# Kernel optimization log

Hardware: AMD Instinct MI355X
Metric: run time of the kernel (lower is better)

The kernel has to match this reference:

```python
import jax, jax.numpy as jnp
import numpy as np

BATCH = 2048      # rays
NINTRS = 256      # samples per ray (intersections has NINTRS+1 t-values)
VALID = 128       # valid samples per ray (mask pattern: first VALID of each ray)
NUM_ATOMS = 256   # grid.data_dim: dictionary size
SH_DIM = 9        # (sh_deg+1)^2, sh_deg=2
DATA_DIM = 3 * SH_DIM + 1  # 28: rgb SH coeffs + sigma
RESOLUTION = 256.0
WHITE_BKGD = True


def sh_basis_deg2(dirs):
    # dirs: (B, 3) -> (B, 9) real SH basis up to degree 2
    d = dirs / jnp.linalg.norm(dirs, axis=-1, keepdims=True)
    x, y, z = d[:, 0], d[:, 1], d[:, 2]
    one = jnp.ones_like(x)
    return jnp.stack([
        0.28209479177387814 * one,
        -0.4886025119029199 * y,
        0.4886025119029199 * z,
        -0.4886025119029199 * x,
        1.0925484305920792 * x * y,
        -1.0925484305920792 * y * z,
        0.31539156525252005 * (2.0 * z * z - x * x - y * y),
        -1.0925484305920792 * x * z,
        0.5462742152960396 * (x * x - y * y),
    ], axis=-1)


def setup_inputs() -> dict:
    key = jax.random.key(0)
    k1, k2, k3, k4, k5 = jax.random.split(key, 5)
    n_pts = BATCH * VALID
    queries = jax.random.normal(k1, (n_pts, NUM_ATOMS), dtype=jnp.float32) * 0.05
    atoms = jax.random.normal(k2, (NUM_ATOMS, DATA_DIM, 8), dtype=jnp.float32) * 0.1
    intrs_pts = jax.random.uniform(k3, (n_pts, 3), minval=-1.0, maxval=1.0, dtype=jnp.float32)
    deltas = jax.random.uniform(k4, (BATCH, NINTRS + 1), minval=0.01, maxval=0.05, dtype=jnp.float32)
    intersections = 2.0 + jnp.cumsum(deltas, axis=-1)  # sorted t-values per ray
    rays_d = jax.random.normal(k5, (BATCH, 3), dtype=jnp.float32)
    rays_d = rays_d / jnp.linalg.norm(rays_d, axis=-1, keepdims=True)
    # mask pattern: first VALID samples of each ray -> flat row-major indices
    b = np.arange(BATCH)[:, None]
    i = np.arange(VALID)[None, :]
    flat_idx = jnp.asarray((b * NINTRS + i).reshape(-1), dtype=jnp.int32)
    return {"queries": queries, "atoms": atoms, "intrs_pts": intrs_pts,
            "intersections": intersections, "rays_d": rays_d, "flat_idx": flat_idx}


def reference(queries, atoms, intrs_pts, intersections, rays_d, flat_idx):
    n_pts = queries.shape[0]
    # sparse-dictionary decode: (n_pts, num_atoms) @ (num_atoms, data_dim*8)
    data_masked = (queries @ atoms.reshape(NUM_ATOMS, -1)).reshape(n_pts, DATA_DIM, 8)

    # trilinear interpolation over the 8 corners (xyzs computed under no_grad)
    pts = jax.lax.stop_gradient(intrs_pts * (RESOLUTION / 2.0) + 1e-05)
    xyzs = pts - jnp.floor(pts)
    x, y, z = xyzs[:, 0], xyzs[:, 1], xyzs[:, 2]
    cx = jnp.stack([1.0 - x, x], axis=-1)  # (n, 2)
    cy = jnp.stack([1.0 - y, y], axis=-1)
    cz = jnp.stack([1.0 - z, z], axis=-1)
    w = (cx[:, :, None, None] * cy[:, None, :, None] * cz[:, None, None, :]).reshape(n_pts, 8)
    data_interp = jnp.einsum('ndc,nc->nd', data_masked, w)  # (n_pts, data_dim)

    # scatter sigma into ray-indexed buffer (masked_scatter_ equivalent)
    sigma_masked = data_interp[:, -1]
    sigma = jnp.zeros((BATCH * NINTRS,), dtype=sigma_masked.dtype).at[flat_idx].set(sigma_masked)
    sigma = jax.nn.relu(sigma.reshape(BATCH, NINTRS))

    # sigma2alpha: alpha compositing weights
    dists = (intersections[:, 1:] - intersections[:, :-1]) * jnp.linalg.norm(rays_d, axis=-1, keepdims=True)
    alpha = 1.0 - jnp.exp(-sigma * dists)
    trans = jnp.cumprod(1.0 - alpha + 1e-10, axis=-1)
    trans = jnp.concatenate([jnp.ones((BATCH, 1), dtype=alpha.dtype), trans[:, :-1]], axis=-1)
    abs_light = alpha * trans  # (batch, nintrs)

    # SH color reconstruction per masked point
    sh_mult_full = sh_basis_deg2(rays_d)                 # (batch, sh_dim)
    ray_idx = flat_idx // NINTRS
    sh_mult = sh_mult_full[ray_idx]                      # (n_pts, sh_dim)
    sh_masked = data_interp[:, :-1].reshape(n_pts, 3, SH_DIM)
    rgb_masked = jnp.sum(sh_mult[:, None, :] * sh_masked, axis=-1)  # (n_pts, 3)
    rgb = jnp.zeros((BATCH * NINTRS, 3), dtype=rgb_masked.dtype).at[flat_idx].set(rgb_masked)
    rgb = rgb.reshape(BATCH, NINTRS, 3)

    # shrgb2rgb: sigmoid + composite (+ white background)
    rgb = jax.nn.sigmoid(rgb)
    rgb = jnp.sum(abs_light[:, :, None] * rgb, axis=1)
    if WHITE_BKGD:
        rgb = rgb + (1.0 - jnp.sum(abs_light, axis=-1, keepdims=True))

    # depth_map: expected t at interval midpoints
    mids = 0.5 * (intersections[:, 1:] + intersections[:, :-1])
    depth = jnp.sum(abs_light * mids, axis=-1)
    return rgb, alpha, depth
```

## Files before the change

kernel.cpp:

```cpp
#include <hip/hip_runtime.h>
#include <hip/hip_bf16.h>
#include <math.h>

#define BATCH   2048
#define NINTRS  256
#define VALID   128
#define NATOMS  256
#define DDIM    28

typedef float  f32x4  __attribute__((ext_vector_type(4)));
typedef short  bf16x8 __attribute__((ext_vector_type(8)));

__device__ __forceinline__ unsigned short f32_to_bf16(float f) {
    unsigned int u = __float_as_uint(f);
    u = (u + 0x7FFFu + ((u >> 16) & 1u)) >> 16;
    return (unsigned short)u;
}

__global__ __launch_bounds__(256)
void build_atomsB(const float* __restrict__ atoms, unsigned short* __restrict__ ab)
{
    const int t = blockIdx.x * 256 + threadIdx.x;
    const int d = t >> 8;
    const int a = t & 255;
    const float* src = atoms + ((size_t)a * DDIM + d) * 8;
    f32x4 v0 = *(const f32x4*)(src);
    f32x4 v1 = *(const f32x4*)(src + 4);
    bf16x8 o;
    #pragma unroll
    for (int j = 0; j < 4; ++j) {
        o[j]   = (short)f32_to_bf16(v0[j]);
        o[j+4] = (short)f32_to_bf16(v1[j]);
    }
    *(bf16x8*)(ab + (size_t)t * 8) = o;
}

__global__ __launch_bounds__(256, 3)
void shdict_fused(const float* __restrict__ q,
                  const unsigned short* __restrict__ ab,
                  const float* __restrict__ ipts,
                  const float* __restrict__ intr,
                  const float* __restrict__ raysd,
                  float* __restrict__ out_rgb,
                  float* __restrict__ out_alpha,
                  float* __restrict__ out_depth)
{
    __shared__ char  bs[32 * 256 * 2];
    __shared__ float w_lds[VALID][9];
    __shared__ float pr_lds[VALID][5];

    const int ray  = blockIdx.x;
    const int tid  = threadIdx.x;
    const int lane = tid & 63;
    const int wav  = tid >> 6;

    const float rdx = raysd[ray*3+0], rdy = raysd[ray*3+1], rdz = raysd[ray*3+2];
    float px = 0.f, py = 0.f, pz = 0.f;
    if (tid < VALID) {
        const int n = ray * VALID + tid;
        px = ipts[n*3+0]*128.0f + 1e-5f;
        py = ipts[n*3+1]*128.0f + 1e-5f;
        pz = ipts[n*3+2]*128.0f + 1e-5f;
    }

    bf16x8 abv[28];
    #pragma unroll
    for (int d = 0; d < 28; ++d)
        abv[d] = *(const bf16x8*)(ab + ((size_t)(d * 256 + tid)) * 8);

    const float ss = rdx*rdx + rdy*rdy + rdz*rdz;
    const float rn = rsqrtf(ss);
    const float x = rdx*rn, y = rdy*rn, z = rdz*rn;
    float sh[9];
    sh[0] = 0.28209479177387814f;
    sh[1] = -0.4886025119029199f * y;
    sh[2] =  0.4886025119029199f * z;
    sh[3] = -0.4886025119029199f * x;
    sh[4] =  1.0925484305920792f * x * y;
    sh[5] = -1.0925484305920792f * y * z;
    sh[6] =  0.31539156525252005f * (2.0f*z*z - x*x - y*y);
    sh[7] = -1.0925484305920792f * x * z;
    sh[8] =  0.5462742152960396f * (x*x - y*y);

    {
        const int a = tid;
        float accB[3][8];
        #pragma unroll
        for (int k = 0; k < 3; ++k)
            #pragma unroll
            for (int c = 0; c < 8; ++c) accB[k][c] = 0.0f;
        #pragma unroll
        for (int d = 0; d < 27; ++d) {
            const int kp = d / 9, j = d - kp * 9;
            const float s = sh[j];
            const unsigned int* u = (const unsigned int*)&abv[d];
            #pragma unroll
            for (int i = 0; i < 4; ++i) {
                const float flo = __uint_as_float(u[i] << 16);
                const float fhi = __uint_as_float(u[i] & 0xffff0000u);
                accB[kp][2*i]   = fmaf(s, flo, accB[kp][2*i]);
                accB[kp][2*i+1] = fmaf(s, fhi, accB[kp][2*i+1]);
            }
        }
        #pragma unroll
        for (int kp = 0; kp < 3; ++kp)
            #pragma unroll
            for (int c = 0; c < 8; ++c) {
                const int col = kp*8 + c;
                unsigned byte = ((unsigned)col << 9) + ((unsigned)a << 1);
                byte ^= (unsigned)((col & 7) << 4);
                *(unsigned short*)(bs + byte) = f32_to_bf16(accB[kp][c]);
            }
        const unsigned short* sv = (const unsigned short*)&abv[27];
        #pragma unroll
        for (int c = 0; c < 8; ++c) {
            const int col = 24 + c;
            unsigned byte = ((unsigned)col << 9) + ((unsigned)a << 1);
            byte ^= (unsigned)((col & 7) << 4);
            *(unsigned short*)(bs + byte) = sv[c];
        }
    }

    if (tid < VALID) {
        const float fx = px - floorf(px);
        const float fy = py - floorf(py);
        const float fz = pz - floorf(pz);
        #pragma unroll
        for (int c = 0; c < 8; ++c) {
            const float wx = (c & 4) ? fx : 1.0f - fx;
            const float wy = (c & 2) ? fy : 1.0f - fy;
            const float wz = (c & 1) ? fz : 1.0f - fz;
            w_lds[tid][c] = wx * wy * wz;
        }
    }

    const int row  = lane & 15;
    const int kgrp = lane >> 4;
    const float* ga0 = q + (size_t)(ray*VALID + wav*32 + row) * NATOMS + kgrp*8;
    const float* ga1 = ga0 + 16 * NATOMS;

    f32x4 pf[3][4];

#define ISSUE_STEP(s, kk) do {                                                   \
    const float* _p0 = ga0 + (kk)*32;                                            \
    const float* _p1 = ga1 + (kk)*32;                                            \
    asm volatile("global_load_dwordx4 %0, %1, off" : "=v"(pf[s][0]) : "v"(_p0)   : "memory"); \
    asm volatile("global_load_dwordx4 %0, %1, off" : "=v"(pf[s][1]) : "v"(_p0+4) : "memory"); \
    asm volatile("global_load_dwordx4 %0, %1, off" : "=v"(pf[s][2]) : "v"(_p1)   : "memory"); \
    asm volatile("global_load_dwordx4 %0, %1, off" : "=v"(pf[s][3]) : "v"(_p1+4) : "memory"); \
} while (0)

    asm volatile("s_waitcnt vmcnt(0)" ::: "memory");
    ISSUE_STEP(0, 0);
    ISSUE_STEP(1, 1);
    ISSUE_STEP(2, 2);

    asm volatile("s_waitcnt lgkmcnt(0)" ::: "memory");
    __builtin_amdgcn_s_barrier();

    f32x4 acc[2][2];
    #pragma unroll
    for (int m = 0; m < 2; ++m)
        #pragma unroll
        for (int n = 0; n < 2; ++n)
            acc[m][n] = (f32x4){0.f, 0.f, 0.f, 0.f};

    #pragma unroll
    for (int ks = 0; ks < 8; ++ks) {
        if (ks <= 5)      asm volatile("s_waitcnt vmcnt(8)" ::: "memory");
        else if (ks == 6) asm volatile("s_waitcnt vmcnt(4)" ::: "memory");
        else              asm volatile("s_waitcnt vmcnt(0)" ::: "memory");
        __builtin_amdgcn_sched_barrier(0);

        const int s = ks % 3;
        bf16x8 af0, af1;
        #pragma unroll
        for (int j = 0; j < 4; ++j) {
            af0[j]   = (short)f32_to_bf16(pf[s][0][j]);
            af0[j+4] = (short)f32_to_bf16(pf[s][1][j]);
            af1[j]   = (short)f32_to_bf16(pf[s][2][j]);
            af1[j+4] = (short)f32_to_bf16(pf[s][3][j]);
        }

        if (ks + 3 < 8) ISSUE_STEP(s, ks + 3);

        bf16x8 bfrag[2];
        const int abase = ks*32 + kgrp*8;
        #pragma unroll
        for (int nt = 0; nt < 2; ++nt) {
            const int col = nt*16 + row;
            unsigned byte = ((unsigned)col << 9) + ((unsigned)abase << 1);
            byte ^= (unsigned)((col & 7) << 4);
            bfrag[nt] = *(const bf16x8*)(bs + byte);
        }

        acc[0][0] = __builtin_amdgcn_mfma_f32_16x16x32_bf16(af0, bfrag[0], acc[0][0], 0, 0, 0);
        acc[0][1] = __builtin_amdgcn_mfma_f32_16x16x32_bf16(af0, bfrag[1], acc[0][1], 0, 0, 0);
        acc[1][0] = __builtin_amdgcn_mfma_f32_16x16x32_bf16(af1, bfrag[0], acc[1][0], 0, 0, 0);
        acc[1][1] = __builtin_amdgcn_mfma_f32_16x16x32_bf16(af1, bfrag[1], acc[1][1], 0, 0, 0);
    }
#undef ISSUE_STEP

    const int cc  = lane & 7;
    const int kph = (lane & 15) >> 3;
    #pragma unroll
    for (int m = 0; m < 2; ++m) {
        const int ptb = wav*32 + m*16 + kgrp*4;
        #pragma unroll
        for (int nt = 0; nt < 2; ++nt) {
            const int kp = nt*2 + kph;
            #pragma unroll
            for (int r = 0; r < 4; ++r) {
                float t = acc[m][nt][r] * w_lds[ptb + r][cc];
                t += __shfl_xor(t, 1);
                t += __shfl_xor(t, 2);
                t += __shfl_xor(t, 4);
                if (cc == 0) pr_lds[ptb + r][kp] = t;
            }
        }
    }
    __syncthreads();

    if (wav == 0) {
        const float rnorm = sqrtf(ss);
        const int i0 = lane * 2;
        const float t0 = intr[ray*257 + i0];
        const float t1 = intr[ray*257 + i0 + 1];
        const float t2 = intr[ray*257 + i0 + 2];
        const float d0 = (t1 - t0) * rnorm;
        const float d1 = (t2 - t1) * rnorm;
        const float s0 = fmaxf(pr_lds[i0][3],     0.0f);
        const float s1 = fmaxf(pr_lds[i0 + 1][3], 0.0f);
        const float a0 = 1.0f - __expf(-s0 * d0);
        const float a1 = 1.0f - __expf(-s1 * d1);
        const float f0 = 1.0f - a0 + 1e-10f;
        const float f1 = 1.0f - a1 + 1e-10f;

        float pprod = f0 * f1;
        #pragma unroll
        for (int off = 1; off < 64; off <<= 1) {
            float v = __shfl_up(pprod, off);
            if (lane >= off) pprod *= v;
        }
        float excl = __shfl_up(pprod, 1);
        if (lane == 0) excl = 1.0f;

        const float tr0 = excl;
        const float tr1 = excl * f0;
        const float al0 = a0 * tr0;
        const float al1 = a1 * tr1;
        const float mid0 = 0.5f * (t0 + t1);
        const float mid1 = 0.5f * (t1 + t2);

        const float r0 = 1.0f / (1.0f + __expf(-pr_lds[i0][0]));
        const float g0 = 1.0f / (1.0f + __expf(-pr_lds[i0][1]));
        const float b0 = 1.0f / (1.0f + __expf(-pr_lds[i0][2]));
        const float r1 = 1.0f / (1.0f + __expf(-pr_lds[i0 + 1][0]));
        const float g1 = 1.0f / (1.0f + __expf(-pr_lds[i0 + 1][1]));
        const float b1 = 1.0f / (1.0f + __expf(-pr_lds[i0 + 1][2]));

        float sum_r = al0*r0 + al1*r1;
        float sum_g = al0*g0 + al1*g1;
        float sum_b = al0*b0 + al1*b1;
        float sum_d = al0*mid0 + al1*mid1;
        float sum_a = al0 + al1;
        #pragma unroll
        for (int off = 1; off < 64; off <<= 1) {
            sum_r += __shfl_xor(sum_r, off);
            sum_g += __shfl_xor(sum_g, off);
            sum_b += __shfl_xor(sum_b, off);
            sum_d += __shfl_xor(sum_d, off);
            sum_a += __shfl_xor(sum_a, off);
        }
        if (lane == 0) {
            const float bkgd = 1.0f - sum_a;
            out_rgb[ray*3 + 0] = sum_r + bkgd;
            out_rgb[ray*3 + 1] = sum_g + bkgd;
            out_rgb[ray*3 + 2] = sum_b + bkgd;
            out_depth[ray]     = sum_d;
        }
        float2 av; av.x = a0; av.y = a1;
        *(float2*)(out_alpha + (size_t)ray*NINTRS + i0) = av;
        float2 zz; zz.x = 0.0f; zz.y = 0.0f;
        *(float2*)(out_alpha + (size_t)ray*NINTRS + VALID + i0) = zz;
    }
}

extern "C" void kernel_launch(void* const* d_in, const int* in_sizes, int n_in,
                              void* d_out, int out_size, void* d_ws, size_t ws_size,
                              hipStream_t stream)
{
    const float* q     = (const float*)d_in[0];
    const float* atoms = (const float*)d_in[1];
    const float* ipts  = (const float*)d_in[2];
    const float* intr  = (const float*)d_in[3];
    const float* raysd = (const float*)d_in[4];

    float* out = (float*)d_out;
    float* out_rgb   = out;
    float* out_alpha = out + BATCH*3;
    float* out_depth = out + BATCH*3 + (size_t)BATCH*NINTRS;

    unsigned short* ab = (unsigned short*)d_ws;

    build_atomsB<<<28, 256, 0, stream>>>(atoms, ab);
    shdict_fused<<<BATCH, 256, 0, stream>>>(q, ab, ipts, intr, raysd,
                                            out_rgb, out_alpha, out_depth);
}
```

Before: 58.81 us.

## Split atom loads into two halves, deepen query prefetch, raise occupancy target

Result: no change. 57.91 us (-1.5%).

```diff
diff --git a/kernel.cpp b/kernel.cpp
--- a/kernel.cpp
+++ b/kernel.cpp
@@ -35,7 +35,7 @@
     *(bf16x8*)(ab + (size_t)t * 8) = o;
 }
 
-__global__ __launch_bounds__(256, 3)
+__global__ __launch_bounds__(256, 4)
 void shdict_fused(const float* __restrict__ q,
                   const unsigned short* __restrict__ ab,
                   const float* __restrict__ ipts,
@@ -63,11 +63,6 @@
         pz = ipts[n*3+2]*128.0f + 1e-5f;
     }
 
-    bf16x8 abv[28];
-    #pragma unroll
-    for (int d = 0; d < 28; ++d)
-        abv[d] = *(const bf16x8*)(ab + ((size_t)(d * 256 + tid)) * 8);
-
     const float ss = rdx*rdx + rdy*rdy + rdz*rdz;
     const float rn = rsqrtf(ss);
     const float x = rdx*rn, y = rdy*rn, z = rdz*rn;
@@ -80,7 +75,20 @@
     sh[5] = -1.0925484305920792f * y * z;
     sh[6] =  0.31539156525252005f * (2.0f*z*z - x*x - y*y);
     sh[7] = -1.0925484305920792f * x * z;
-    sh[8] =  0.5462742152960396f * (x*x - y*y);
+    sh[8] =  0.5462742152960396f * (x-y)*(x+y);
+
+    if (tid < VALID) {
+        const float fx = px - floorf(px);
+        const float fy = py - floorf(py);
+        const float fz = pz - floorf(pz);
+        #pragma unroll
+        for (int c = 0; c < 8; ++c) {
+            const float wx = (c & 4) ? fx : 1.0f - fx;
+            const float wy = (c & 2) ? fy : 1.0f - fy;
+            const float wz = (c & 1) ? fz : 1.0f - fz;
+            w_lds[tid][c] = wx * wy * wz;
+        }
+    }
 
     {
         const int a = tid;
@@ -89,11 +97,16 @@
         for (int k = 0; k < 3; ++k)
             #pragma unroll
             for (int c = 0; c < 8; ++c) accB[k][c] = 0.0f;
-        #pragma unroll
-        for (int d = 0; d < 27; ++d) {
+
+        bf16x8 h[14];
+        #pragma unroll
+        for (int d = 0; d < 14; ++d)
+            h[d] = *(const bf16x8*)(ab + ((size_t)(d * 256 + a)) * 8);
+        #pragma unroll
+        for (int d = 0; d < 14; ++d) {
             const int kp = d / 9, j = d - kp * 9;
             const float s = sh[j];
-            const unsigned int* u = (const unsigned int*)&abv[d];
+            const unsigned int* u = (const unsigned int*)&h[d];
             #pragma unroll
             for (int i = 0; i < 4; ++i) {
                 const float flo = __uint_as_float(u[i] << 16);
@@ -102,6 +115,24 @@
                 accB[kp][2*i+1] = fmaf(s, fhi, accB[kp][2*i+1]);
             }
         }
+        __builtin_amdgcn_sched_barrier(0);
+        #pragma unroll
+        for (int d = 0; d < 14; ++d)
+            h[d] = *(const bf16x8*)(ab + ((size_t)((d + 14) * 256 + a)) * 8);
+        #pragma unroll
+        for (int d = 0; d < 13; ++d) {
+            const int dd = d + 14;
+            const int kp = dd / 9, j = dd - kp * 9;
+            const float s = sh[j];
+            const unsigned int* u = (const unsigned int*)&h[d];
+            #pragma unroll
+            for (int i = 0; i < 4; ++i) {
+                const float flo = __uint_as_float(u[i] << 16);
+                const float fhi = __uint_as_float(u[i] & 0xffff0000u);
+                accB[kp][2*i]   = fmaf(s, flo, accB[kp][2*i]);
+                accB[kp][2*i+1] = fmaf(s, fhi, accB[kp][2*i+1]);
+            }
+        }
         #pragma unroll
         for (int kp = 0; kp < 3; ++kp)
             #pragma unroll
@@ -111,7 +142,7 @@
                 byte ^= (unsigned)((col & 7) << 4);
                 *(unsigned short*)(bs + byte) = f32_to_bf16(accB[kp][c]);
             }
-        const unsigned short* sv = (const unsigned short*)&abv[27];
+        const unsigned short* sv = (const unsigned short*)&h[13];
         #pragma unroll
         for (int c = 0; c < 8; ++c) {
             const int col = 24 + c;
@@ -121,25 +152,12 @@
         }
     }
 
-    if (tid < VALID) {
-        const float fx = px - floorf(px);
-        const float fy = py - floorf(py);
-        const float fz = pz - floorf(pz);
-        #pragma unroll
-        for (int c = 0; c < 8; ++c) {
-            const float wx = (c & 4) ? fx : 1.0f - fx;
-            const float wy = (c & 2) ? fy : 1.0f - fy;
-            const float wz = (c & 1) ? fz : 1.0f - fz;
-            w_lds[tid][c] = wx * wy * wz;
-        }
-    }
-
     const int row  = lane & 15;
     const int kgrp = lane >> 4;
     const float* ga0 = q + (size_t)(ray*VALID + wav*32 + row) * NATOMS + kgrp*8;
     const float* ga1 = ga0 + 16 * NATOMS;
 
-    f32x4 pf[3][4];
+    f32x4 pf[4][4];
 
 #define ISSUE_STEP(s, kk) do {                                                   \
     const float* _p0 = ga0 + (kk)*32;                                            \
@@ -154,6 +172,7 @@
     ISSUE_STEP(0, 0);
     ISSUE_STEP(1, 1);
     ISSUE_STEP(2, 2);
+    ISSUE_STEP(3, 3);
 
     asm volatile("s_waitcnt lgkmcnt(0)" ::: "memory");
     __builtin_amdgcn_s_barrier();
@@ -167,12 +186,13 @@
 
     #pragma unroll
     for (int ks = 0; ks < 8; ++ks) {
-        if (ks <= 5)      asm volatile("s_waitcnt vmcnt(8)" ::: "memory");
-        else if (ks == 6) asm volatile("s_waitcnt vmcnt(4)" ::: "memory");
-        else              asm volatile("s_waitcnt vmcnt(0)" ::: "memory");
+        if (ks <= 4)      asm volatile("s_waitcnt vmcnt(12)" ::: "memory");
+        else if (ks == 5) asm volatile("s_waitcnt vmcnt(8)"  ::: "memory");
+        else if (ks == 6) asm volatile("s_waitcnt vmcnt(4)"  ::: "memory");
+        else              asm volatile("s_waitcnt vmcnt(0)"  ::: "memory");
         __builtin_amdgcn_sched_barrier(0);
 
-        const int s = ks % 3;
+        const int s = ks & 3;
         bf16x8 af0, af1;
         #pragma unroll
         for (int j = 0; j < 4; ++j) {
@@ -182,7 +202,7 @@
             af1[j+4] = (short)f32_to_bf16(pf[s][3][j]);
         }
 
-        if (ks + 3 < 8) ISSUE_STEP(s, ks + 3);
+        if (ks + 4 < 8) ISSUE_STEP(s, ks + 4);
 
         bf16x8 bfrag[2];
         const int abase = ks*32 + kgrp*8;
```

## Precompute per-ray SH-projected B tiles in separate kernel and async-load into LDS

Applied to the files above, without the earlier changes.

Measured after the change: 75.82 us. +28.9%, slower.

```diff
diff --git a/kernel.cpp b/kernel.cpp
--- a/kernel.cpp
+++ b/kernel.cpp
@@ -35,55 +35,35 @@
     *(bf16x8*)(ab + (size_t)t * 8) = o;
 }
 
-__global__ __launch_bounds__(256, 3)
-void shdict_fused(const float* __restrict__ q,
-                  const unsigned short* __restrict__ ab,
-                  const float* __restrict__ ipts,
-                  const float* __restrict__ intr,
+__global__ __launch_bounds__(256)
+void build_bs_all(const unsigned short* __restrict__ ab,
                   const float* __restrict__ raysd,
-                  float* __restrict__ out_rgb,
-                  float* __restrict__ out_alpha,
-                  float* __restrict__ out_depth)
+                  unsigned short* __restrict__ bst)
 {
-    __shared__ char  bs[32 * 256 * 2];
-    __shared__ float w_lds[VALID][9];
-    __shared__ float pr_lds[VALID][5];
-
-    const int ray  = blockIdx.x;
-    const int tid  = threadIdx.x;
-    const int lane = tid & 63;
-    const int wav  = tid >> 6;
-
-    const float rdx = raysd[ray*3+0], rdy = raysd[ray*3+1], rdz = raysd[ray*3+2];
-    float px = 0.f, py = 0.f, pz = 0.f;
-    if (tid < VALID) {
-        const int n = ray * VALID + tid;
-        px = ipts[n*3+0]*128.0f + 1e-5f;
-        py = ipts[n*3+1]*128.0f + 1e-5f;
-        pz = ipts[n*3+2]*128.0f + 1e-5f;
-    }
+    const int a = threadIdx.x;
+    const int rbase = blockIdx.x * 8;
 
     bf16x8 abv[28];
     #pragma unroll
     for (int d = 0; d < 28; ++d)
-        abv[d] = *(const bf16x8*)(ab + ((size_t)(d * 256 + tid)) * 8);
-
-    const float ss = rdx*rdx + rdy*rdy + rdz*rdz;
-    const float rn = rsqrtf(ss);
-    const float x = rdx*rn, y = rdy*rn, z = rdz*rn;
-    float sh[9];
-    sh[0] = 0.28209479177387814f;
-    sh[1] = -0.4886025119029199f * y;
-    sh[2] =  0.4886025119029199f * z;
-    sh[3] = -0.4886025119029199f * x;
-    sh[4] =  1.0925484305920792f * x * y;
-    sh[5] = -1.0925484305920792f * y * z;
-    sh[6] =  0.31539156525252005f * (2.0f*z*z - x*x - y*y);
-    sh[7] = -1.0925484305920792f * x * z;
-    sh[8] =  0.5462742152960396f * (x*x - y*y);
-
-    {
-        const int a = tid;
+        abv[d] = *(const bf16x8*)(ab + ((size_t)(d * 256 + a)) * 8);
+
+    for (int r = 0; r < 8; ++r) {
+        const int ray = rbase + r;
+        const float rdx = raysd[ray*3+0], rdy = raysd[ray*3+1], rdz = raysd[ray*3+2];
+        const float rn = rsqrtf(rdx*rdx + rdy*rdy + rdz*rdz);
+        const float x = rdx*rn, y = rdy*rn, z = rdz*rn;
+        float sh[9];
+        sh[0] = 0.28209479177387814f;
+        sh[1] = -0.4886025119029199f * y;
+        sh[2] =  0.4886025119029199f * z;
+        sh[3] = -0.4886025119029199f * x;
+        sh[4] =  1.0925484305920792f * x * y;
+        sh[5] = -1.0925484305920792f * y * z;
+        sh[6] =  0.31539156525252005f * (2.0f*z*z - x*x - y*y);
+        sh[7] = -1.0925484305920792f * x * z;
+        sh[8] =  0.5462742152960396f * (x - y) * (x + y);
+
         float accB[3][8];
         #pragma unroll
         for (int k = 0; k < 3; ++k)
@@ -102,6 +82,8 @@
                 accB[kp][2*i+1] = fmaf(s, fhi, accB[kp][2*i+1]);
             }
         }
+
+        char* ob = (char*)bst + (size_t)ray * 16384;
         #pragma unroll
         for (int kp = 0; kp < 3; ++kp)
             #pragma unroll
@@ -109,7 +91,7 @@
                 const int col = kp*8 + c;
                 unsigned byte = ((unsigned)col << 9) + ((unsigned)a << 1);
                 byte ^= (unsigned)((col & 7) << 4);
-                *(unsigned short*)(bs + byte) = f32_to_bf16(accB[kp][c]);
+                *(unsigned short*)(ob + byte) = f32_to_bf16(accB[kp][c]);
             }
         const unsigned short* sv = (const unsigned short*)&abv[27];
         #pragma unroll
@@ -117,11 +99,37 @@
             const int col = 24 + c;
             unsigned byte = ((unsigned)col << 9) + ((unsigned)a << 1);
             byte ^= (unsigned)((col & 7) << 4);
-            *(unsigned short*)(bs + byte) = sv[c];
-        }
-    }
-
+            *(unsigned short*)(ob + byte) = sv[c];
+        }
+    }
+}
+
+__global__ __launch_bounds__(256, 4)
+void shdict_fused(const float* __restrict__ q,
+                  const unsigned short* __restrict__ bst,
+                  const float* __restrict__ ipts,
+                  const float* __restrict__ intr,
+                  const float* __restrict__ raysd,
+                  float* __restrict__ out_rgb,
+                  float* __restrict__ out_alpha,
+                  float* __restrict__ out_depth)
+{
+    __shared__ char  bs[32 * 256 * 2];
+    __shared__ float w_lds[VALID][9];
+    __shared__ float pr_lds[VALID][5];
+
+    const int ray  = blockIdx.x;
+    const int tid  = threadIdx.x;
+    const int lane = tid & 63;
+    const int wav  = tid >> 6;
+
+    const float rdx = raysd[ray*3+0], rdy = raysd[ray*3+1], rdz = raysd[ray*3+2];
+    const float ss  = rdx*rdx + rdy*rdy + rdz*rdz;
     if (tid < VALID) {
+        const int n = ray * VALID + tid;
+        const float px = ipts[n*3+0]*128.0f + 1e-5f;
+        const float py = ipts[n*3+1]*128.0f + 1e-5f;
+        const float pz = ipts[n*3+2]*128.0f + 1e-5f;
         const float fx = px - floorf(px);
         const float fy = py - floorf(py);
         const float fz = pz - floorf(pz);
@@ -133,13 +141,27 @@
             w_lds[tid][c] = wx * wy * wz;
         }
     }
+    asm volatile("s_waitcnt vmcnt(0)" ::: "memory");
+
+    {
+        const char* gbs = (const char*)bst + (size_t)ray * 16384
+                        + (size_t)wav * 1024 + (size_t)lane * 16;
+        char* lbs = (char*)bs + wav * 1024;
+        #pragma unroll
+        for (int j = 0; j < 4; ++j) {
+            __builtin_amdgcn_global_load_lds(
+                (const __attribute__((address_space(1))) void*)(gbs + j * 4096),
+                (__attribute__((address_space(3))) void*)(lbs + j * 4096),
+                16, 0, 0);
+        }
+    }
 
     const int row  = lane & 15;
     const int kgrp = lane >> 4;
     const float* ga0 = q + (size_t)(ray*VALID + wav*32 + row) * NATOMS + kgrp*8;
     const float* ga1 = ga0 + 16 * NATOMS;
 
-    f32x4 pf[3][4];
+    f32x4 pf[4][4];
 
 #define ISSUE_STEP(s, kk) do {                                                   \
     const float* _p0 = ga0 + (kk)*32;                                            \
@@ -150,10 +172,10 @@
     asm volatile("global_load_dwordx4 %0, %1, off" : "=v"(pf[s][3]) : "v"(_p1+4) : "memory"); \
 } while (0)
 
-    asm volatile("s_waitcnt vmcnt(0)" ::: "memory");
     ISSUE_STEP(0, 0);
     ISSUE_STEP(1, 1);
     ISSUE_STEP(2, 2);
+    ISSUE_STEP(3, 3);
 
     asm volatile("s_waitcnt lgkmcnt(0)" ::: "memory");
     __builtin_amdgcn_s_barrier();
@@ -167,12 +189,13 @@
 
     #pragma unroll
     for (int ks = 0; ks < 8; ++ks) {
-        if (ks <= 5)      asm volatile("s_waitcnt vmcnt(8)" ::: "memory");
-        else if (ks == 6) asm volatile("s_waitcnt vmcnt(4)" ::: "memory");
-        else              asm volatile("s_waitcnt vmcnt(0)" ::: "memory");
+        if (ks <= 4)      asm volatile("s_waitcnt vmcnt(12)" ::: "memory");
+        else if (ks == 5) asm volatile("s_waitcnt vmcnt(8)"  ::: "memory");
+        else if (ks == 6) asm volatile("s_waitcnt vmcnt(4)"  ::: "memory");
+        else              asm volatile("s_waitcnt vmcnt(0)"  ::: "memory");
         __builtin_amdgcn_sched_barrier(0);
 
-        const int s = ks % 3;
+        const int s = ks & 3;
         bf16x8 af0, af1;
         #pragma unroll
         for (int j = 0; j < 4; ++j) {
@@ -182,7 +205,7 @@
             af1[j+4] = (short)f32_to_bf16(pf[s][3][j]);
         }
 
-        if (ks + 3 < 8) ISSUE_STEP(s, ks + 3);
+        if (ks + 4 < 8) ISSUE_STEP(s, ks + 4);
 
         bf16x8 bfrag[2];
         const int abase = ks*32 + kgrp*8;
@@ -301,9 +324,11 @@
     float* out_alpha = out + BATCH*3;
     float* out_depth = out + BATCH*3 + (size_t)BATCH*NINTRS;
 
-    unsigned short* ab = (unsigned short*)d_ws;
+    unsigned short* ab  = (unsigned short*)d_ws;
+    unsigned short* bst = (unsigned short*)((char*)d_ws + (1 << 20));
 
     build_atomsB<<<28, 256, 0, stream>>>(atoms, ab);
-    shdict_fused<<<BATCH, 256, 0, stream>>>(q, ab, ipts, intr, raysd,
+    build_bs_all<<<BATCH/8, 256, 0, stream>>>(ab, raysd, bst);
+    shdict_fused<<<BATCH, 256, 0, stream>>>(q, bst, ipts, intr, raysd,
                                             out_rgb, out_alpha, out_depth);
 }
```
